# Performance work log

Measured on AMD Instinct MI355X. Metric: run time of the kernel, lower is better.

Reference implementation:

```python
import jax, jax.numpy as jnp
import numpy as np

N_NODES = 100000
N_EDGES = 1600000
DIMS = [256, 128, 64, 32, 16]  # halving pyramid from number_of_x=256 down to number_of_classes=16
N_LAYERS = len(DIMS) - 1


def setup_inputs() -> dict:
    key = jax.random.key(0)
    ks = jax.random.split(key, 3 + N_LAYERS)
    inp = {
        "x": jax.random.normal(ks[0], (N_NODES, DIMS[0]), jnp.float32),
        "src": jax.random.randint(ks[1], (N_EDGES,), 0, N_NODES),
        "dst": jax.random.randint(ks[2], (N_EDGES,), 0, N_NODES),
    }
    for i in range(N_LAYERS):
        inp[f"W{i}"] = jax.random.normal(ks[3 + i], (DIMS[i], DIMS[i + 1]), jnp.float32) / np.sqrt(DIMS[i])
        inp[f"b{i}"] = jnp.zeros((DIMS[i + 1],), jnp.float32)   # GraphConv bias
        inp[f"sb{i}"] = jnp.zeros((1,), jnp.float32)            # module's extra scalar bias
    return inp


def _gcn_layer(h, src, dst, W, b, norm_src, norm_dst):
    # DGL GraphConv, norm='both', in_feats >= out_feats -> transform first, then aggregate
    h = h * norm_src[:, None]                                    # D_out^{-1/2} * X
    h = h @ W                                                    # GEMM
    agg = jax.ops.segment_sum(h[src], dst, num_segments=N_NODES) # SpMM aggregation
    return agg * norm_dst[:, None] + b                           # D_in^{-1/2}, + bias


def reference(x, src, dst, W0, b0, sb0, W1, b1, sb1, W2, b2, sb2, W3, b3, sb3):
    ones = jnp.ones((N_EDGES,), jnp.float32)
    out_deg = jax.ops.segment_sum(ones, src, num_segments=N_NODES)
    in_deg = jax.ops.segment_sum(ones, dst, num_segments=N_NODES)
    norm_src = jnp.maximum(out_deg, 1.0) ** -0.5
    norm_dst = jnp.maximum(in_deg, 1.0) ** -0.5
    h = x
    for W, b, sb in ((W0, b0, sb0), (W1, b1, sb1), (W2, b2, sb2), (W3, b3, sb3)):
        h = jax.nn.relu(_gcn_layer(h, src, dst, W, b, norm_src, norm_dst) + sb)
    return jax.nn.softmax(h, axis=1)
```

## Files before the change

kernel.cpp:

```cpp
#include <hip/hip_runtime.h>
#include <hip/hip_bf16.h>

#define N_NODES 100000
#define N_EDGES 1600000
#define NSHARD 4

typedef unsigned short u16;
typedef unsigned int u32;

static __device__ __forceinline__ u16 f2bf(float f) {
    union { float f; u32 u; } v; v.f = f;
    u32 u = v.u;
    u += 0x7FFFu + ((u >> 16) & 1u);
    return (u16)(u >> 16);
}
static __device__ __forceinline__ float bf2f(u16 h) {
    union { float f; u32 u; } v; v.u = ((u32)h) << 16; return v.f;
}

__global__ __launch_bounds__(256) void degree_kernel(
    const int* __restrict__ src, const int* __restrict__ dst,
    u32* __restrict__ shist, u32* __restrict__ dhist, u32* __restrict__ pos) {
    int e = blockIdx.x * 256 + threadIdx.x;
    if (e < N_EDGES) {
        int sh = threadIdx.x >> 6;
        atomicAdd(&shist[sh * N_NODES + src[e]], 1u);
        pos[e] = atomicAdd(&dhist[sh * N_NODES + dst[e]], 1u);
    }
}

__global__ __launch_bounds__(256) void csr_prep_kernel(
    u32* __restrict__ dhist, const u32* __restrict__ shist,
    u32* __restrict__ indeg, float* __restrict__ norm_src, float* __restrict__ norm_dst) {
    int n = blockIdx.x * 256 + threadIdx.x;
    if (n >= N_NODES) return;
    u32 d0 = dhist[n], d1 = dhist[N_NODES + n], d2 = dhist[2 * N_NODES + n], d3 = dhist[3 * N_NODES + n];
    u32 s0 = shist[n], s1 = shist[N_NODES + n], s2 = shist[2 * N_NODES + n], s3 = shist[3 * N_NODES + n];
    u32 id = d0 + d1 + d2 + d3;
    u32 od = s0 + s1 + s2 + s3;
    indeg[n] = id;
    norm_dst[n] = rsqrtf((float)(id < 1u ? 1u : id));
    norm_src[n] = rsqrtf((float)(od < 1u ? 1u : od));
    dhist[n] = 0u;
    dhist[N_NODES + n] = d0;
    dhist[2 * N_NODES + n] = d0 + d1;
    dhist[3 * N_NODES + n] = d0 + d1 + d2;
}

#define SCAN_B 512
#define SCAN_NBLK ((N_NODES + SCAN_B - 1) / SCAN_B)

__global__ __launch_bounds__(SCAN_B) void scan1_kernel(
    const u32* __restrict__ indeg, u32* __restrict__ row_ptr, u32* __restrict__ bsum) {
    __shared__ u32 s[SCAN_B];
    int t = threadIdx.x;
    int gid = blockIdx.x * SCAN_B + t;
    u32 v = (gid < N_NODES) ? indeg[gid] : 0u;
    s[t] = v;
    __syncthreads();
    for (int off = 1; off < SCAN_B; off <<= 1) {
        u32 x = (t >= off) ? s[t - off] : 0u;
        __syncthreads();
        s[t] += x;
        __syncthreads();
    }
    if (gid < N_NODES) row_ptr[gid + 1] = s[t];
    if (t == SCAN_B - 1) bsum[blockIdx.x] = s[t];
}

__global__ __launch_bounds__(256) void scan2_kernel(u32* __restrict__ bsum, u32* __restrict__ boff) {
    __shared__ u32 s[256];
    int t = threadIdx.x;
    s[t] = (t < SCAN_NBLK) ? bsum[t] : 0u;
    __syncthreads();
    for (int off = 1; off < 256; off <<= 1) {
        u32 x = (t >= off) ? s[t - off] : 0u;
        __syncthreads();
        s[t] += x;
        __syncthreads();
    }
    if (t < SCAN_NBLK) boff[t] = (t == 0) ? 0u : s[t - 1];
}

__global__ __launch_bounds__(256) void scan3_kernel(u32* __restrict__ row_ptr, const u32* __restrict__ boff) {
    int gid = blockIdx.x * 256 + threadIdx.x;
    if (gid < N_NODES) {
        row_ptr[gid + 1] += boff[gid / SCAN_B];
        if (gid == 0) row_ptr[0] = 0u;
    }
}

__global__ __launch_bounds__(256) void fill_kernel(
    const int* __restrict__ src, const int* __restrict__ dst,
    const u32* __restrict__ row_ptr, const u32* __restrict__ base,
    const u32* __restrict__ pos, u32* __restrict__ col) {
    int e = blockIdx.x * 256 + threadIdx.x;
    if (e < N_EDGES) {
        int d = dst[e];
        int sh = threadIdx.x >> 6;
        u32 p = row_ptr[d] + base[sh * N_NODES + d] + pos[e];
        col[p] = (u32)src[e];
    }
}

template <int DIN, int DOUT>
__global__ __launch_bounds__(256) void gemm_kernel(
    const float* __restrict__ h, const float* __restrict__ W,
    const float* __restrict__ norm_src, u16* __restrict__ T) {
    constexpr int TM = 64;
    constexpr int KT = 32;
    constexpr int JBLKS = DOUT / 4;
    constexpr int NPT = (TM * DOUT) / (256 * 4);

    __shared__ float hs[KT][TM + 4];
    __shared__ float ws[KT][DOUT];

    const int t = threadIdx.x;
    const int m0 = blockIdx.x * TM;
    const int jblk = t % JBLKS;
    const int nblk = t / JBLKS;
    const int n0 = nblk * NPT;

    float acc[NPT][4];
    for (int i = 0; i < NPT; ++i)
        for (int j = 0; j < 4; ++j) acc[i][j] = 0.f;

    for (int k0 = 0; k0 < DIN; k0 += KT) {
        for (int it = 0; it < 2; ++it) {
            int f = t + it * 256;
            int row = f / (KT / 4);
            int c4  = f % (KT / 4);
            float4 v = make_float4(0.f, 0.f, 0.f, 0.f);
            int gr = m0 + row;
            if (gr < N_NODES)
                v = *reinterpret_cast<const float4*>(&h[gr * DIN + k0 + c4 * 4]);
            hs[c4 * 4 + 0][row] = v.x;
            hs[c4 * 4 + 1][row] = v.y;
            hs[c4 * 4 + 2][row] = v.z;
            hs[c4 * 4 + 3][row] = v.w;
        }
        constexpr int WQ = KT * DOUT / 4;
        constexpr int WITERS = (WQ + 255) / 256;
        for (int it = 0; it < WITERS; ++it) {
            int f = t + it * 256;
            if (f < WQ) {
                int row = f / JBLKS;
                int c4  = f % JBLKS;
                *reinterpret_cast<float4*>(&ws[row][c4 * 4]) =
                    *reinterpret_cast<const float4*>(&W[(k0 + row) * DOUT + c4 * 4]);
            }
        }
        __syncthreads();

#pragma unroll 4
        for (int k = 0; k < KT; ++k) {
            float4 wv = *reinterpret_cast<const float4*>(&ws[k][jblk * 4]);
            float a[NPT];
            if constexpr (NPT % 4 == 0) {
#pragma unroll
                for (int i = 0; i < NPT; i += 4)
                    *reinterpret_cast<float4*>(&a[i]) =
                        *reinterpret_cast<const float4*>(&hs[k][n0 + i]);
            } else if constexpr (NPT == 2) {
                *reinterpret_cast<float2*>(&a[0]) =
                    *reinterpret_cast<const float2*>(&hs[k][n0]);
            } else {
                a[0] = hs[k][n0];
            }
#pragma unroll
            for (int i = 0; i < NPT; ++i) {
                acc[i][0] = fmaf(a[i], wv.x, acc[i][0]);
                acc[i][1] = fmaf(a[i], wv.y, acc[i][1]);
                acc[i][2] = fmaf(a[i], wv.z, acc[i][2]);
                acc[i][3] = fmaf(a[i], wv.w, acc[i][3]);
            }
        }
        __syncthreads();
    }

#pragma unroll
    for (int i = 0; i < NPT; ++i) {
        int n = m0 + n0 + i;
        if (n < N_NODES) {
            float s = norm_src[n];
            ushort4 o;
            o.x = f2bf(acc[i][0] * s);
            o.y = f2bf(acc[i][1] * s);
            o.z = f2bf(acc[i][2] * s);
            o.w = f2bf(acc[i][3] * s);
            *reinterpret_cast<ushort4*>(&T[n * DOUT + jblk * 4]) = o;
        }
    }
}

template <int D>
__global__ __launch_bounds__(256) void pull_kernel(
    const u16* __restrict__ T, const u32* __restrict__ row_ptr,
    const u32* __restrict__ col, const float* __restrict__ norm_dst,
    const float* __restrict__ b, const float* __restrict__ sb,
    float* __restrict__ h) {
    constexpr int TPN = D / 4;
    int tid = blockIdx.x * 256 + threadIdx.x;
    int n = tid / TPN;
    int c = (tid % TPN) * 4;
    if (n >= N_NODES) return;

    u32 beg = row_ptr[n], end = row_ptr[n + 1];
    float a0 = 0.f, a1 = 0.f, a2 = 0.f, a3 = 0.f;

    u32 e = beg;
    for (; e + 1 < end; e += 2) {
        u32 s0 = col[e], s1 = col[e + 1];
        ushort4 v0 = *reinterpret_cast<const ushort4*>(&T[s0 * D + c]);
        ushort4 v1 = *reinterpret_cast<const ushort4*>(&T[s1 * D + c]);
        a0 += bf2f(v0.x) + bf2f(v1.x);
        a1 += bf2f(v0.y) + bf2f(v1.y);
        a2 += bf2f(v0.z) + bf2f(v1.z);
        a3 += bf2f(v0.w) + bf2f(v1.w);
    }
    if (e < end) {
        u32 s0 = col[e];
        ushort4 v0 = *reinterpret_cast<const ushort4*>(&T[s0 * D + c]);
        a0 += bf2f(v0.x); a1 += bf2f(v0.y); a2 += bf2f(v0.z); a3 += bf2f(v0.w);
    }

    float nd = norm_dst[n];
    float sv = sb[0];
    float4 bb = *reinterpret_cast<const float4*>(&b[c]);
    float4 o;
    o.x = fmaxf(a0 * nd + bb.x + sv, 0.f);
    o.y = fmaxf(a1 * nd + bb.y + sv, 0.f);
    o.z = fmaxf(a2 * nd + bb.z + sv, 0.f);
    o.w = fmaxf(a3 * nd + bb.w + sv, 0.f);
    *reinterpret_cast<float4*>(&h[n * D + c]) = o;
}

__global__ __launch_bounds__(256) void softmax_kernel(
    const float* __restrict__ h, float* __restrict__ out) {
    int n = blockIdx.x * 256 + threadIdx.x;
    if (n >= N_NODES) return;
    float v[16];
#pragma unroll
    for (int j4 = 0; j4 < 4; ++j4) {
        float4 a = *reinterpret_cast<const float4*>(&h[n * 16 + j4 * 4]);
        v[j4 * 4 + 0] = a.x; v[j4 * 4 + 1] = a.y;
        v[j4 * 4 + 2] = a.z; v[j4 * 4 + 3] = a.w;
    }
    float m = v[0];
#pragma unroll
    for (int j = 1; j < 16; ++j) m = fmaxf(m, v[j]);
    float sum = 0.f;
#pragma unroll
    for (int j = 0; j < 16; ++j) { v[j] = __expf(v[j] - m); sum += v[j]; }
    float inv = 1.f / sum;
    float* op = out + n * 16;
#pragma unroll
    for (int j4 = 0; j4 < 4; ++j4) {
        float4 o = make_float4(v[j4 * 4 + 0] * inv, v[j4 * 4 + 1] * inv,
                               v[j4 * 4 + 2] * inv, v[j4 * 4 + 3] * inv);
        *reinterpret_cast<float4*>(op + j4 * 4) = o;
    }
}

extern "C" void kernel_launch(void* const* d_in, const int* in_sizes, int n_in,
                              void* d_out, int out_size, void* d_ws, size_t ws_size,
                              hipStream_t stream) {
    const float* x   = (const float*)d_in[0];
    const int*   src = (const int*)d_in[1];
    const int*   dst = (const int*)d_in[2];
    const float* W0 = (const float*)d_in[3];
    const float* b0 = (const float*)d_in[4];
    const float* sb0 = (const float*)d_in[5];
    const float* W1 = (const float*)d_in[6];
    const float* b1 = (const float*)d_in[7];
    const float* sb1 = (const float*)d_in[8];
    const float* W2 = (const float*)d_in[9];
    const float* b2 = (const float*)d_in[10];
    const float* sb2 = (const float*)d_in[11];
    const float* W3 = (const float*)d_in[12];
    const float* b3 = (const float*)d_in[13];
    const float* sb3 = (const float*)d_in[14];

    char* ws = (char*)d_ws;
    float* h        = (float*)ws;
    u16*   T        = (u16*)(ws + 51200000);
    u32*   dhist    = (u32*)(ws + 51200000);
    u32*   shist    = (u32*)(ws + 51200000 + 1600000);
    u32*   pos      = (u32*)(ws + 51200000 + 3200000);
    u32*   col      = (u32*)(ws + 76800000);
    u32*   row_ptr  = (u32*)(ws + 83200000);
    float* norm_src = (float*)(ws + 83600016);
    float* norm_dst = (float*)(ws + 84000016);
    u32*   bsum     = (u32*)(ws + 84400016);
    u32*   boff     = (u32*)(ws + 84404016);
    u32*   indeg    = (u32*)(ws + 84408016);

    const int EB = (N_EDGES + 255) / 256;
    const int NB = (N_NODES + 255) / 256;
    const int MT = (N_NODES + 63) / 64;

    hipMemsetAsync(dhist, 0, 2 * NSHARD * N_NODES * 4, stream);
    degree_kernel<<<EB, 256, 0, stream>>>(src, dst, shist, dhist, pos);
    csr_prep_kernel<<<NB, 256, 0, stream>>>(dhist, shist, indeg, norm_src, norm_dst);
    scan1_kernel<<<SCAN_NBLK, SCAN_B, 0, stream>>>(indeg, row_ptr, bsum);
    scan2_kernel<<<1, 256, 0, stream>>>(bsum, boff);
    scan3_kernel<<<NB, 256, 0, stream>>>(row_ptr, boff);
    fill_kernel<<<EB, 256, 0, stream>>>(src, dst, row_ptr, dhist, pos, col);

    gemm_kernel<256, 128><<<MT, 256, 0, stream>>>(x, W0, norm_src, T);
    pull_kernel<128><<<(N_NODES * 32 + 255) / 256, 256, 0, stream>>>(T, row_ptr, col, norm_dst, b0, sb0, h);

    gemm_kernel<128, 64><<<MT, 256, 0, stream>>>(h, W1, norm_src, T);
    pull_kernel<64><<<(N_NODES * 16 + 255) / 256, 256, 0, stream>>>(T, row_ptr, col, norm_dst, b1, sb1, h);

    gemm_kernel<64, 32><<<MT, 256, 0, stream>>>(h, W2, norm_src, T);
    pull_kernel<32><<<(N_NODES * 8 + 255) / 256, 256, 0, stream>>>(T, row_ptr, col, norm_dst, b2, sb2, h);

    gemm_kernel<32, 16><<<MT, 256, 0, stream>>>(h, W3, norm_src, T);
    pull_kernel<16><<<(N_NODES * 4 + 255) / 256, 256, 0, stream>>>(T, row_ptr, col, norm_dst, b3, sb3, h);
    softmax_kernel<<<NB, 256, 0, stream>>>(h, (float*)d_out);
}
```

Before: 646.6 us.

## Widen pull gathers to 16B, fuse softmax into last layer, drop sharded histograms

The pull kernels now have each thread gather 8 bf16 values (16-byte loads) instead of 4, halving the thread count per node. The final layer's aggregation is fused with the softmax so the intermediate h write and the separate softmax pass go away. The degree histograms also drop their 4-way sharding, which removes the csr_prep merge pass, at the cost of more atomic contention on the single histogram.

```diff
diff --git a/kernel.cpp b/kernel.cpp
--- a/kernel.cpp
+++ b/kernel.cpp
@@ -3,7 +3,6 @@
 
 #define N_NODES 100000
 #define N_EDGES 1600000
-#define NSHARD 4
 
 typedef unsigned short u16;
 typedef unsigned int u32;
@@ -14,8 +13,11 @@
     u += 0x7FFFu + ((u >> 16) & 1u);
     return (u16)(u >> 16);
 }
-static __device__ __forceinline__ float bf2f(u16 h) {
-    union { float f; u32 u; } v; v.u = ((u32)h) << 16; return v.f;
+static __device__ __forceinline__ float bflo(u32 w) {
+    union { u32 u; float f; } v; v.u = w << 16; return v.f;
+}
+static __device__ __forceinline__ float bfhi(u32 w) {
+    union { u32 u; float f; } v; v.u = w & 0xFFFF0000u; return v.f;
 }
 
 __global__ __launch_bounds__(256) void degree_kernel(
@@ -23,28 +25,19 @@
     u32* __restrict__ shist, u32* __restrict__ dhist, u32* __restrict__ pos) {
     int e = blockIdx.x * 256 + threadIdx.x;
     if (e < N_EDGES) {
-        int sh = threadIdx.x >> 6;
-        atomicAdd(&shist[sh * N_NODES + src[e]], 1u);
-        pos[e] = atomicAdd(&dhist[sh * N_NODES + dst[e]], 1u);
-    }
-}
-
-__global__ __launch_bounds__(256) void csr_prep_kernel(
-    u32* __restrict__ dhist, const u32* __restrict__ shist,
-    u32* __restrict__ indeg, float* __restrict__ norm_src, float* __restrict__ norm_dst) {
+        atomicAdd(&shist[src[e]], 1u);
+        pos[e] = atomicAdd(&dhist[dst[e]], 1u);
+    }
+}
+
+__global__ __launch_bounds__(256) void norm_kernel(
+    const u32* __restrict__ dhist, const u32* __restrict__ shist,
+    float* __restrict__ norm_src, float* __restrict__ norm_dst) {
     int n = blockIdx.x * 256 + threadIdx.x;
     if (n >= N_NODES) return;
-    u32 d0 = dhist[n], d1 = dhist[N_NODES + n], d2 = dhist[2 * N_NODES + n], d3 = dhist[3 * N_NODES + n];
-    u32 s0 = shist[n], s1 = shist[N_NODES + n], s2 = shist[2 * N_NODES + n], s3 = shist[3 * N_NODES + n];
-    u32 id = d0 + d1 + d2 + d3;
-    u32 od = s0 + s1 + s2 + s3;
-    indeg[n] = id;
+    u32 id = dhist[n], od = shist[n];
     norm_dst[n] = rsqrtf((float)(id < 1u ? 1u : id));
     norm_src[n] = rsqrtf((float)(od < 1u ? 1u : od));
-    dhist[n] = 0u;
-    dhist[N_NODES + n] = d0;
-    dhist[2 * N_NODES + n] = d0 + d1;
-    dhist[3 * N_NODES + n] = d0 + d1 + d2;
 }
 
 #define SCAN_B 512
@@ -92,14 +85,12 @@
 
 __global__ __launch_bounds__(256) void fill_kernel(
     const int* __restrict__ src, const int* __restrict__ dst,
-    const u32* __restrict__ row_ptr, const u32* __restrict__ base,
-    const u32* __restrict__ pos, u32* __restrict__ col) {
+    const u32* __restrict__ row_ptr, const u32* __restrict__ pos,
+    u32* __restrict__ col) {
     int e = blockIdx.x * 256 + threadIdx.x;
     if (e < N_EDGES) {
         int d = dst[e];
-        int sh = threadIdx.x >> 6;
-        u32 p = row_ptr[d] + base[sh * N_NODES + d] + pos[e];
-        col[p] = (u32)src[e];
+        col[row_ptr[d] + pos[e]] = (u32)src[e];
     }
 }
 
@@ -199,67 +190,120 @@
     const u32* __restrict__ col, const float* __restrict__ norm_dst,
     const float* __restrict__ b, const float* __restrict__ sb,
     float* __restrict__ h) {
-    constexpr int TPN = D / 4;
+    constexpr int TPN = D / 8;
     int tid = blockIdx.x * 256 + threadIdx.x;
     int n = tid / TPN;
-    int c = (tid % TPN) * 4;
+    int c = (tid % TPN) * 8;
     if (n >= N_NODES) return;
 
     u32 beg = row_ptr[n], end = row_ptr[n + 1];
-    float a0 = 0.f, a1 = 0.f, a2 = 0.f, a3 = 0.f;
+    float a[8];
+#pragma unroll
+    for (int j = 0; j < 8; ++j) a[j] = 0.f;
 
     u32 e = beg;
     for (; e + 1 < end; e += 2) {
         u32 s0 = col[e], s1 = col[e + 1];
-        ushort4 v0 = *reinterpret_cast<const ushort4*>(&T[s0 * D + c]);
-        ushort4 v1 = *reinterpret_cast<const ushort4*>(&T[s1 * D + c]);
-        a0 += bf2f(v0.x) + bf2f(v1.x);
-        a1 += bf2f(v0.y) + bf2f(v1.y);
-        a2 += bf2f(v0.z) + bf2f(v1.z);
-        a3 += bf2f(v0.w) + bf2f(v1.w);
+        uint4 q0 = *reinterpret_cast<const uint4*>(&T[s0 * D + c]);
+        uint4 q1 = *reinterpret_cast<const uint4*>(&T[s1 * D + c]);
+        a[0] += bflo(q0.x) + bflo(q1.x);
+        a[1] += bfhi(q0.x) + bfhi(q1.x);
+        a[2] += bflo(q0.y) + bflo(q1.y);
+        a[3] += bfhi(q0.y) + bfhi(q1.y);
+        a[4] += bflo(q0.z) + bflo(q1.z);
+        a[5] += bfhi(q0.z) + bfhi(q1.z);
+        a[6] += bflo(q0.w) + bflo(q1.w);
+        a[7] += bfhi(q0.w) + bfhi(q1.w);
     }
     if (e < end) {
-        u32 s0 = col[e];
-        ushort4 v0 = *reinterpret_cast<const ushort4*>(&T[s0 * D + c]);
-        a0 += bf2f(v0.x); a1 += bf2f(v0.y); a2 += bf2f(v0.z); a3 += bf2f(v0.w);
+        uint4 q0 = *reinterpret_cast<const uint4*>(&T[col[e] * D + c]);
+        a[0] += bflo(q0.x); a[1] += bfhi(q0.x);
+        a[2] += bflo(q0.y); a[3] += bfhi(q0.y);
+        a[4] += bflo(q0.z); a[5] += bfhi(q0.z);
+        a[6] += bflo(q0.w); a[7] += bfhi(q0.w);
     }
 
     float nd = norm_dst[n];
     float sv = sb[0];
-    float4 bb = *reinterpret_cast<const float4*>(&b[c]);
-    float4 o;
-    o.x = fmaxf(a0 * nd + bb.x + sv, 0.f);
-    o.y = fmaxf(a1 * nd + bb.y + sv, 0.f);
-    o.z = fmaxf(a2 * nd + bb.z + sv, 0.f);
-    o.w = fmaxf(a3 * nd + bb.w + sv, 0.f);
-    *reinterpret_cast<float4*>(&h[n * D + c]) = o;
-}
-
-__global__ __launch_bounds__(256) void softmax_kernel(
-    const float* __restrict__ h, float* __restrict__ out) {
-    int n = blockIdx.x * 256 + threadIdx.x;
+    float4 b0 = *reinterpret_cast<const float4*>(&b[c]);
+    float4 b1 = *reinterpret_cast<const float4*>(&b[c + 4]);
+    float4 o0, o1;
+    o0.x = fmaxf(a[0] * nd + b0.x + sv, 0.f);
+    o0.y = fmaxf(a[1] * nd + b0.y + sv, 0.f);
+    o0.z = fmaxf(a[2] * nd + b0.z + sv, 0.f);
+    o0.w = fmaxf(a[3] * nd + b0.w + sv, 0.f);
+    o1.x = fmaxf(a[4] * nd + b1.x + sv, 0.f);
+    o1.y = fmaxf(a[5] * nd + b1.y + sv, 0.f);
+    o1.z = fmaxf(a[6] * nd + b1.z + sv, 0.f);
+    o1.w = fmaxf(a[7] * nd + b1.w + sv, 0.f);
+    *reinterpret_cast<float4*>(&h[n * D + c])     = o0;
+    *reinterpret_cast<float4*>(&h[n * D + c + 4]) = o1;
+}
+
+__global__ __launch_bounds__(256) void pull16_sm_kernel(
+    const u16* __restrict__ T, const u32* __restrict__ row_ptr,
+    const u32* __restrict__ col, const float* __restrict__ norm_dst,
+    const float* __restrict__ b, const float* __restrict__ sb,
+    float* __restrict__ out) {
+    int tid = blockIdx.x * 256 + threadIdx.x;
+    int n = tid >> 1;
+    int c = (tid & 1) * 8;
     if (n >= N_NODES) return;
-    float v[16];
-#pragma unroll
-    for (int j4 = 0; j4 < 4; ++j4) {
-        float4 a = *reinterpret_cast<const float4*>(&h[n * 16 + j4 * 4]);
-        v[j4 * 4 + 0] = a.x; v[j4 * 4 + 1] = a.y;
-        v[j4 * 4 + 2] = a.z; v[j4 * 4 + 3] = a.w;
-    }
-    float m = v[0];
-#pragma unroll
-    for (int j = 1; j < 16; ++j) m = fmaxf(m, v[j]);
-    float sum = 0.f;
-#pragma unroll
-    for (int j = 0; j < 16; ++j) { v[j] = __expf(v[j] - m); sum += v[j]; }
-    float inv = 1.f / sum;
-    float* op = out + n * 16;
-#pragma unroll
-    for (int j4 = 0; j4 < 4; ++j4) {
-        float4 o = make_float4(v[j4 * 4 + 0] * inv, v[j4 * 4 + 1] * inv,
-                               v[j4 * 4 + 2] * inv, v[j4 * 4 + 3] * inv);
-        *reinterpret_cast<float4*>(op + j4 * 4) = o;
-    }
+
+    u32 beg = row_ptr[n], end = row_ptr[n + 1];
+    float a[8];
+#pragma unroll
+    for (int j = 0; j < 8; ++j) a[j] = 0.f;
+
+    u32 e = beg;
+    for (; e + 1 < end; e += 2) {
+        u32 s0 = col[e], s1 = col[e + 1];
+        uint4 q0 = *reinterpret_cast<const uint4*>(&T[s0 * 16 + c]);
+        uint4 q1 = *reinterpret_cast<const uint4*>(&T[s1 * 16 + c]);
+        a[0] += bflo(q0.x) + bflo(q1.x);
+        a[1] += bfhi(q0.x) + bfhi(q1.x);
+        a[2] += bflo(q0.y) + bflo(q1.y);
+        a[3] += bfhi(q0.y) + bfhi(q1.y);
+        a[4] += bflo(q0.z) + bflo(q1.z);
+        a[5] += bfhi(q0.z) + bfhi(q1.z);
+        a[6] += bflo(q0.w) + bflo(q1.w);
+        a[7] += bfhi(q0.w) + bfhi(q1.w);
+    }
+    if (e < end) {
+        uint4 q0 = *reinterpret_cast<const uint4*>(&T[col[e] * 16 + c]);
+        a[0] += bflo(q0.x); a[1] += bfhi(q0.x);
+        a[2] += bflo(q0.y); a[3] += bfhi(q0.y);
+        a[4] += bflo(q0.z); a[5] += bfhi(q0.z);
+        a[6] += bflo(q0.w); a[7] += bfhi(q0.w);
+    }
+
+    float nd = norm_dst[n];
+    float sv = sb[0];
+    float4 b0 = *reinterpret_cast<const float4*>(&b[c]);
+    float4 b1 = *reinterpret_cast<const float4*>(&b[c + 4]);
+    float o[8];
+    o[0] = fmaxf(a[0] * nd + b0.x + sv, 0.f);
+    o[1] = fmaxf(a[1] * nd + b0.y + sv, 0.f);
+    o[2] = fmaxf(a[2] * nd + b0.z + sv, 0.f);
+    o[3] = fmaxf(a[3] * nd + b0.w + sv, 0.f);
+    o[4] = fmaxf(a[4] * nd + b1.x + sv, 0.f);
+    o[5] = fmaxf(a[5] * nd + b1.y + sv, 0.f);
+    o[6] = fmaxf(a[6] * nd + b1.z + sv, 0.f);
+    o[7] = fmaxf(a[7] * nd + b1.w + sv, 0.f);
+
+    float m = o[0];
+#pragma unroll
+    for (int j = 1; j < 8; ++j) m = fmaxf(m, o[j]);
+    m = fmaxf(m, __shfl_xor(m, 1));
+    float s = 0.f;
+#pragma unroll
+    for (int j = 0; j < 8; ++j) { o[j] = __expf(o[j] - m); s += o[j]; }
+    s += __shfl_xor(s, 1);
+    float inv = 1.f / s;
+    float4 w0 = make_float4(o[0] * inv, o[1] * inv, o[2] * inv, o[3] * inv);
+    float4 w1 = make_float4(o[4] * inv, o[5] * inv, o[6] * inv, o[7] * inv);
+    *reinterpret_cast<float4*>(&out[n * 16 + c])     = w0;
+    *reinterpret_cast<float4*>(&out[n * 16 + c + 4]) = w1;
 }
 
 extern "C" void kernel_launch(void* const* d_in, const int* in_sizes, int n_in,
@@ -285,38 +329,36 @@
     float* h        = (float*)ws;
     u16*   T        = (u16*)(ws + 51200000);
     u32*   dhist    = (u32*)(ws + 51200000);
-    u32*   shist    = (u32*)(ws + 51200000 + 1600000);
-    u32*   pos      = (u32*)(ws + 51200000 + 3200000);
+    u32*   shist    = (u32*)(ws + 51600000);
+    u32*   pos      = (u32*)(ws + 52000000);
     u32*   col      = (u32*)(ws + 76800000);
     u32*   row_ptr  = (u32*)(ws + 83200000);
     float* norm_src = (float*)(ws + 83600016);
     float* norm_dst = (float*)(ws + 84000016);
     u32*   bsum     = (u32*)(ws + 84400016);
     u32*   boff     = (u32*)(ws + 84404016);
-    u32*   indeg    = (u32*)(ws + 84408016);
 
     const int EB = (N_EDGES + 255) / 256;
     const int NB = (N_NODES + 255) / 256;
     const int MT = (N_NODES + 63) / 64;
 
-    hipMemsetAsync(dhist, 0, 2 * NSHARD * N_NODES * 4, stream);
+    hipMemsetAsync(dhist, 0, 2 * N_NODES * 4, stream);
     degree_kernel<<<EB, 256, 0, stream>>>(src, dst, shist, dhist, pos);
-    csr_prep_kernel<<<NB, 256, 0, stream>>>(dhist, shist, indeg, norm_src, norm_dst);
-    scan1_kernel<<<SCAN_NBLK, SCAN_B, 0, stream>>>(indeg, row_ptr, bsum);
+    norm_kernel<<<NB, 256, 0, stream>>>(dhist, shist, norm_src, norm_dst);
+    scan1_kernel<<<SCAN_NBLK, SCAN_B, 0, stream>>>(dhist, row_ptr, bsum);
     scan2_kernel<<<1, 256, 0, stream>>>(bsum, boff);
     scan3_kernel<<<NB, 256, 0, stream>>>(row_ptr, boff);
-    fill_kernel<<<EB, 256, 0, stream>>>(src, dst, row_ptr, dhist, pos, col);
+    fill_kernel<<<EB, 256, 0, stream>>>(src, dst, row_ptr, pos, col);
 
     gemm_kernel<256, 128><<<MT, 256, 0, stream>>>(x, W0, norm_src, T);
-    pull_kernel<128><<<(N_NODES * 32 + 255) / 256, 256, 0, stream>>>(T, row_ptr, col, norm_dst, b0, sb0, h);
+    pull_kernel<128><<<(N_NODES * 16 + 255) / 256, 256, 0, stream>>>(T, row_ptr, col, norm_dst, b0, sb0, h);
 
     gemm_kernel<128, 64><<<MT, 256, 0, stream>>>(h, W1, norm_src, T);
-    pull_kernel<64><<<(N_NODES * 16 + 255) / 256, 256, 0, stream>>>(T, row_ptr, col, norm_dst, b1, sb1, h);
+    pull_kernel<64><<<(N_NODES * 8 + 255) / 256, 256, 0, stream>>>(T, row_ptr, col, norm_dst, b1, sb1, h);
 
     gemm_kernel<64, 32><<<MT, 256, 0, stream>>>(h, W2, norm_src, T);
-    pull_kernel<32><<<(N_NODES * 8 + 255) / 256, 256, 0, stream>>>(T, row_ptr, col, norm_dst, b2, sb2, h);
+    pull_kernel<32><<<(N_NODES * 4 + 255) / 256, 256, 0, stream>>>(T, row_ptr, col, norm_dst, b2, sb2, h);
 
     gemm_kernel<32, 16><<<MT, 256, 0, stream>>>(h, W3, norm_src, T);
-    pull_kernel<16><<<(N_NODES * 4 + 255) / 256, 256, 0, stream>>>(T, row_ptr, col, norm_dst, b3, sb3, h);
-    softmax_kernel<<<NB, 256, 0, stream>>>(h, (float*)d_out);
-}
+    pull16_sm_kernel<<<(N_NODES * 2 + 255) / 256, 256, 0, stream>>>(T, row_ptr, col, norm_dst, b3, sb3, (float*)d_out);
+}
```

Result: faster. 617.3 us (-4.5%).
